# Kernel optimization log

Measured on AMD Instinct MI355X. Metric: run time of the kernel, lower is better.

The kernel has to match this reference:

```python
import jax, jax.numpy as jnp
import numpy as np

BS, H, W, C = 32, 64, 64, 256
SEQ = 32


def setup_inputs() -> dict:
    key = jax.random.key(0)
    k1, k2, k3, k4, k5 = jax.random.split(key, 5)
    x = jax.random.normal(k1, (BS, H, W, C), dtype=jnp.float32)
    sentence = jax.random.normal(k2, (BS, C), dtype=jnp.float32)  # unused in call()
    context = jax.random.normal(k3, (BS, SEQ, C), dtype=jnp.float32)
    mask = jax.random.bernoulli(k4, 0.3, (BS, SEQ))
    W_word = jax.random.normal(k5, (C, C), dtype=jnp.float32) * (1.0 / np.sqrt(C))
    return {"x": x, "sentence": sentence, "context": context, "mask": mask, "W_word": W_word}


def reference(x, sentence, context, mask, W_word):
    bs, h, w, c = x.shape
    hw = h * w
    seq = context.shape[1]
    xf = x.reshape(bs, hw, c)                                   # [bs, hw, C]
    ctx = jnp.einsum('bsd,dc->bsc', context, W_word)            # conv1x1 word projection
    attn = jnp.einsum('bnc,bsc->bns', xf, ctx)                  # [bs, hw, seq]
    attn = attn.reshape(bs * hw, seq)
    # faithful to original: mask tiled hw times along axis 0 (block-repeat order)
    mask_t = jnp.tile(mask, (hw, 1))                            # [bs*hw, seq]
    neg_inf = jnp.asarray(-jnp.inf, dtype=attn.dtype)
    attn = jnp.where(mask_t, neg_inf, attn)
    attn = jax.nn.softmax(attn, axis=-1).reshape(bs, hw, seq)
    # matmul(ctx^T, attn^T) -> [bs, C, hw] -> transpose -> [bs, hw, C]
    weighted_context = jnp.einsum('bsc,bns->bnc', ctx, attn).reshape(bs, h, w, c)
    word_attn = attn.reshape(bs, h, w, seq)
    return weighted_context, word_attn
```

## Files before the change

### kernel.cpp

```cpp
#include <hip/hip_runtime.h>
#include <stdint.h>

typedef __attribute__((ext_vector_type(8))) short short8;
typedef __attribute__((ext_vector_type(4))) float float4v;

#define HW   4096
#define CC   256
#define SEQQ 32
#define BSZ  32
#define RPB  128

#define SGRP     1032
#define CTXT_SZ  (8 * SGRP)
#define PSTR_P   40

static __device__ __forceinline__ uint16_t f2bf(float f) {
  union { float f; uint32_t u; } v; v.f = f;
  uint32_t r = v.u + 0x7FFFu + ((v.u >> 16) & 1u);
  return (uint16_t)(r >> 16);
}
static __device__ __forceinline__ float bf2f(uint16_t h) {
  union { uint32_t u; float f; } v; v.u = ((uint32_t)h) << 16;
  return v.f;
}

extern "C" __global__ __launch_bounds__(256) void prep_kernel(
    const float* __restrict__ ctx_in,
    const float* __restrict__ Wp,
    const void*  __restrict__ mask,
    uint32_t* __restrict__ maskbits_ws,
    uint16_t* __restrict__ hiT_ws,
    uint16_t* __restrict__ loT_ws)
{
  const int t = threadIdx.x;
  if (blockIdx.x == 256) {
    __shared__ int byteFlag;
    if (t == 0) byteFlag = 0;
    __syncthreads();
    const uint8_t* mb = (const uint8_t*)mask;
    int nz = 0;
    for (int i = t; i < 1024; i += 256)
      if ((i & 3) == 1 && mb[i] != 0) nz = 1;
    if (nz) atomicOr(&byteFlag, 1);
    __syncthreads();
    const bool byteMode = (byteFlag != 0);
    const uint32_t* mw32 = (const uint32_t*)mask;
    if (t < 32) {
      uint32_t bits = 0;
      for (int s = 0; s < 32; ++s) {
        bool m = byteMode ? (mb[t * 32 + s] != 0) : (mw32[t * 32 + s] != 0);
        if (m) bits |= (1u << s);
      }
      maskbits_ws[t] = bits;
    }
    return;
  }

  const int r0 = blockIdx.x * 4;
  __shared__ float crow[4][CC];
  for (int i = t; i < 1024; i += 256)
    crow[i >> 8][i & 255] = ctx_in[(size_t)r0 * CC + i];
  __syncthreads();

  const int j  = t >> 6;
  const int c4 = (t & 63) << 2;
  float4v acc = {0.f, 0.f, 0.f, 0.f};
  #pragma unroll 8
  for (int d = 0; d < CC; ++d) {
    float s = crow[j][d];
    const float4 wv = *(const float4*)&Wp[(size_t)d * CC + c4];
    acc[0] += s * wv.x; acc[1] += s * wv.y;
    acc[2] += s * wv.z; acc[3] += s * wv.w;
  }

  const int row = r0 + j, bb = row >> 5, ss = row & 31;
  const size_t base = (size_t)bb * CTXT_SZ + (ss >> 2) * SGRP + (ss & 3) * 16;
  #pragma unroll
  for (int q = 0; q < 4; ++q) {
    const int c = c4 + q;
    const float v = acc[q];
    const uint16_t h  = f2bf(v);
    const uint16_t lo = f2bf(v - bf2f(h));
    const size_t idx = base + (c >> 4) * 64 + (c & 15);
    hiT_ws[idx] = h;
    loT_ws[idx] = lo;
  }
}

#define COMPUTE_TILE(XA, XB, TBASE)                                           \
  {                                                                           \
    float4v acc0 = {0.f, 0.f, 0.f, 0.f};                                      \
    float4v acc1 = {0.f, 0.f, 0.f, 0.f};                                      \
    _Pragma("unroll")                                                         \
    for (int k0 = 0; k0 < 8; ++k0) {                                          \
      float xv[8] = {XA[k0].x, XA[k0].y, XA[k0].z, XA[k0].w,                  \
                     XB[k0].x, XB[k0].y, XB[k0].z, XB[k0].w};                 \
      short8 ah, al;                                                          \
      _Pragma("unroll")                                                       \
      for (int jj = 0; jj < 8; ++jj) {                                        \
        uint32_t u = __float_as_uint(xv[jj]);                                 \
        ah[jj] = (short)(u >> 16);                                            \
        float rr_ = xv[jj] - __uint_as_float(u & 0xFFFF0000u);                \
        al[jj] = (short)(__float_as_uint(rr_) >> 16);                         \
      }                                                                       \
      const int ka = sbase + k0 * 128;                                        \
      short8 bh0 = *(const short8*)&hiT[ka];                                  \
      short8 bl0 = *(const short8*)&loT[ka];                                  \
      short8 bh1 = *(const short8*)&hiT[ka + 4 * SGRP];                       \
      short8 bl1 = *(const short8*)&loT[ka + 4 * SGRP];                       \
      acc0 = __builtin_amdgcn_mfma_f32_16x16x32_bf16(bh0, ah, acc0, 0, 0, 0); \
      acc0 = __builtin_amdgcn_mfma_f32_16x16x32_bf16(bl0, ah, acc0, 0, 0, 0); \
      acc0 = __builtin_amdgcn_mfma_f32_16x16x32_bf16(bh0, al, acc0, 0, 0, 0); \
      acc1 = __builtin_amdgcn_mfma_f32_16x16x32_bf16(bh1, ah, acc1, 0, 0, 0); \
      acc1 = __builtin_amdgcn_mfma_f32_16x16x32_bf16(bl1, ah, acc1, 0, 0, 0); \
      acc1 = __builtin_amdgcn_mfma_f32_16x16x32_bf16(bh1, al, acc1, 0, 0, 0); \
    }                                                                         \
    const int n = (TBASE) + l15;                                              \
    const uint32_t mwd = maskW[n & 31];                                       \
    float v[8];                                                               \
    _Pragma("unroll")                                                         \
    for (int r = 0; r < 4; ++r) {                                             \
      v[r]     = (mwd & (1u << (quad * 4 + r)))      ? -1e30f : acc0[r];      \
      v[4 + r] = (mwd & (1u << (16 + quad * 4 + r))) ? -1e30f : acc1[r];      \
    }                                                                         \
    float mx = v[0];                                                          \
    _Pragma("unroll")                                                         \
    for (int jq = 1; jq < 8; ++jq) mx = fmaxf(mx, v[jq]);                     \
    mx = fmaxf(mx, __shfl_xor(mx, 16, 64));                                   \
    mx = fmaxf(mx, __shfl_xor(mx, 32, 64));                                   \
    float e[8], sm = 0.f;                                                     \
    _Pragma("unroll")                                                         \
    for (int jq = 0; jq < 8; ++jq) { e[jq] = __expf(v[jq] - mx); sm += e[jq]; } \
    sm += __shfl_xor(sm, 16, 64);                                             \
    sm += __shfl_xor(sm, 32, 64);                                             \
    const float inv = 1.0f / sm;                                              \
    float p[8];                                                               \
    _Pragma("unroll")                                                         \
    for (int jq = 0; jq < 8; ++jq) p[jq] = e[jq] * inv;                       \
         \
    const int r8 = l15 & 7;                                                   \
    *(float4*)&ostW[l15 * 32 + ((quad ^ r8) << 2)] =                          \
        make_float4(p[0], p[1], p[2], p[3]);                                  \
    *(float4*)&ostW[l15 * 32 + (((4 + quad) ^ r8) << 2)] =                    \
        make_float4(p[4], p[5], p[6], p[7]);                                  \
    uint32_t w0 = (uint32_t)f2bf(p[0]) | ((uint32_t)f2bf(p[1]) << 16);        \
    uint32_t w1 = (uint32_t)f2bf(p[2]) | ((uint32_t)f2bf(p[3]) << 16);        \
    uint32_t w2 = (uint32_t)f2bf(p[4]) | ((uint32_t)f2bf(p[5]) << 16);        \
    uint32_t w3 = (uint32_t)f2bf(p[6]) | ((uint32_t)f2bf(p[7]) << 16);        \
    uint16_t* prow = &pL[(w * 16 + l15) * PSTR_P];                            \
    *(uint2*)(prow + quad * 4)      = make_uint2(w0, w1);                     \
    *(uint2*)(prow + 16 + quad * 4) = make_uint2(w2, w3);                     \
    _Pragma("unroll")                                                         \
    for (int i2 = 0; i2 < 2; ++i2) {                                          \
      const int rr = 8 * i2 + (lane >> 3);                                    \
      const int mm = lane & 7;                                                \
      float4 vv = *(const float4*)&ostW[rr * 32 + ((mm ^ (rr & 7)) << 2)];    \
      *(float4*)(out1 + ((size_t)b * HW + (TBASE) + rr) * SEQQ + mm * 4) = vv;\
    }                                                                         \
     \
    short8 pa = *(const short8*)&pL[(w * 16 + l15) * PSTR_P + quad * 8];      \
    _Pragma("unroll")                                                         \
    for (int cg = 0; cg < 4; ++cg) {                                          \
      _Pragma("unroll")                                                       \
      for (int j2 = 0; j2 < 4; ++j2) {                                        \
        const int ct = cg * 4 + j2;                                           \
        short8 bfr;                                                           \
        _Pragma("unroll")                                                     \
        for (int jj = 0; jj < 8; ++jj)                                        \
          bfr[jj] = (short)hiT[cbase + (jj >> 2) * SGRP + ct * 64 + (jj & 3) * 16]; \
        float4v z = {0.f, 0.f, 0.f, 0.f};                                     \
        float4v dd = __builtin_amdgcn_mfma_f32_16x16x32_bf16(bfr, pa, z, 0, 0, 0); \
        const int ss = j2 * 4 + quad;                                         \
        *(float4*)&ostW[l15 * 64 + ((ss ^ l15) << 2)] =                       \
            make_float4(dd[0], dd[1], dd[2], dd[3]);                          \
      }                                                                       \
      _Pragma("unroll")                                                       \
      for (int i2 = 0; i2 < 4; ++i2) {                                        \
        const int rr = 4 * i2 + (lane >> 4);                                  \
        const int mm = lane & 15;                                             \
        float4 vv = *(const float4*)&ostW[rr * 64 + ((mm ^ rr) << 2)];        \
        *(float4*)(out0 + ((size_t)b * HW + (TBASE) + rr) * CC + cg * 64 + mm * 4) = vv; \
      }                                                                       \
    }                                                                         \
  }

extern "C" __global__ __launch_bounds__(256, 2) void attn_main(
    const float* __restrict__ x,
    const uint8_t* __restrict__ ws,
    float* __restrict__ out0,
    float* __restrict__ out1)
{
  const uint32_t* maskbits_ws = (const uint32_t*)ws;
  const uint16_t* hiT_ws = (const uint16_t*)(ws + 128);
  const uint16_t* loT_ws = hiT_ws + (size_t)BSZ * CTXT_SZ;

  __shared__ __align__(16) uint16_t hiT[CTXT_SZ];
  __shared__ __align__(16) uint16_t loT[CTXT_SZ];
  __shared__ __align__(16) uint16_t pL[64 * PSTR_P];
  __shared__ __align__(16) float    oStgF[4 * 1024];
  __shared__ uint32_t maskW[32];

  const int tid = threadIdx.x;
  const int b   = blockIdx.y;
  const int n0  = blockIdx.x * RPB;

  const int w    = tid >> 6;
  const int lane = tid & 63;
  const int l15  = lane & 15;
  const int quad = lane >> 4;
  const int nwave = n0 + w * 32;
  float* ostW = &oStgF[w * 1024];

  const uint4* sHi = (const uint4*)(hiT_ws + (size_t)b * CTXT_SZ);
  const uint4* sLo = (const uint4*)(loT_ws + (size_t)b * CTXT_SZ);

  uint4 hS[4], lS[4];
  #pragma unroll
  for (int k = 0; k < 4; ++k) {
    hS[k] = sHi[tid + k * 256];
    lS[k] = sLo[tid + k * 256];
  }

  const float* xrow0 = x + ((size_t)b * HW + nwave + l15) * CC + quad * 8;
  float4 xa0[8], xb0[8];
  #pragma unroll
  for (int k0 = 0; k0 < 8; ++k0) {
    xa0[k0] = *(const float4*)(xrow0 + k0 * 32);
    xb0[k0] = *(const float4*)(xrow0 + k0 * 32 + 4);
  }
  asm volatile("" ::: "memory");

  {
    uint4* dHi = (uint4*)hiT;
    uint4* dLo = (uint4*)loT;
    #pragma unroll
    for (int k = 0; k < 4; ++k) {
      dHi[tid + k * 256] = hS[k];
      dLo[tid + k * 256] = lS[k];
    }
    if (tid < 8) { dHi[1024 + tid] = sHi[1024 + tid]; dLo[1024 + tid] = sLo[1024 + tid]; }
    if (tid < 32) maskW[tid] = maskbits_ws[tid];
  }
  __syncthreads();

  const float* xrow1 = xrow0 + 16 * CC;
  float4 xa1[8], xb1[8];
  #pragma unroll
  for (int k0 = 0; k0 < 8; ++k0) {
    xa1[k0] = *(const float4*)(xrow1 + k0 * 32);
    xb1[k0] = *(const float4*)(xrow1 + k0 * 32 + 4);
  }
  asm volatile("" ::: "memory");

  const int sbase = (l15 >> 2) * SGRP + (l15 & 3) * 16 + (quad >> 1) * 64 + (quad & 1) * 8;
  const int cbase = quad * 2 * SGRP + l15;

  COMPUTE_TILE(xa0, xb0, nwave);
  COMPUTE_TILE(xa1, xb1, nwave + 16);
}

extern "C" void kernel_launch(void* const* d_in, const int* in_sizes, int n_in,
                              void* d_out, int out_size, void* d_ws, size_t ws_size,
                              hipStream_t stream) {
  const float* x      = (const float*)d_in[0];
  const float* ctx_in = (const float*)d_in[2];
  const void*  mask   = d_in[3];
  const float* Wp     = (const float*)d_in[4];

  float* out0 = (float*)d_out;
  float* out1 = out0 + (size_t)BSZ * HW * CC;

  uint8_t*  ws          = (uint8_t*)d_ws;
  uint32_t* maskbits_ws = (uint32_t*)ws;
  uint16_t* hiT_ws      = (uint16_t*)(ws + 128);
  uint16_t* loT_ws      = hiT_ws + (size_t)BSZ * CTXT_SZ;

  prep_kernel<<<257, 256, 0, stream>>>(ctx_in, Wp, mask, maskbits_ws,
                                       hiT_ws, loT_ws);
  attn_main<<<dim3(HW / RPB, BSZ), 256, 0, stream>>>(x, ws, out0, out1);
}
```

Before: 281.1 us.

## Double rows per block with software-pipelined x loads and nontemporal stores

Each block now covers 256 rows, and each wave processes four 16-row tiles instead of two. The x loads for the next tile are issued before the current tile is computed, in a double-buffered register pipeline. This spreads the per-block cost of staging the context into shared memory over more rows and overlaps global loads with compute. Output stores switch to nontemporal builtins so they avoid polluting the cache. The change halves the grid size, which may lower occupancy and parallelism, and keeps register pressure high.

```diff
diff --git a/kernel.cpp b/kernel.cpp
--- a/kernel.cpp
+++ b/kernel.cpp
@@ -8,7 +8,7 @@
 #define CC   256
 #define SEQQ 32
 #define BSZ  32
-#define RPB  128
+#define RPB  256
 
 #define SGRP     1032
 #define CTXT_SZ  (8 * SGRP)
@@ -87,6 +87,17 @@
   }
 }
 
+#define LOAD_CHUNK(XA, XB, CIDX)                                              \
+  {                                                                           \
+    const float* xr_ = xrow0 + (CIDX) * 16 * CC;                              \
+    _Pragma("unroll")                                                         \
+    for (int k0 = 0; k0 < 8; ++k0) {                                          \
+      XA[k0] = *(const float4*)(xr_ + k0 * 32);                               \
+      XB[k0] = *(const float4*)(xr_ + k0 * 32 + 4);                           \
+    }                                                                         \
+  }                                                                           \
+  asm volatile("" ::: "memory");
+
 #define COMPUTE_TILE(XA, XB, TBASE)                                           \
   {                                                                           \
     float4v acc0 = {0.f, 0.f, 0.f, 0.f};                                      \
@@ -139,10 +150,10 @@
     for (int jq = 0; jq < 8; ++jq) p[jq] = e[jq] * inv;                       \
          \
     const int r8 = l15 & 7;                                                   \
-    *(float4*)&ostW[l15 * 32 + ((quad ^ r8) << 2)] =                          \
-        make_float4(p[0], p[1], p[2], p[3]);                                  \
-    *(float4*)&ostW[l15 * 32 + (((4 + quad) ^ r8) << 2)] =                    \
-        make_float4(p[4], p[5], p[6], p[7]);                                  \
+    float4v p03 = {p[0], p[1], p[2], p[3]};                                   \
+    float4v p47 = {p[4], p[5], p[6], p[7]};                                   \
+    *(float4v*)&ostW[l15 * 32 + ((quad ^ r8) << 2)]       = p03;              \
+    *(float4v*)&ostW[l15 * 32 + (((4 + quad) ^ r8) << 2)] = p47;              \
     uint32_t w0 = (uint32_t)f2bf(p[0]) | ((uint32_t)f2bf(p[1]) << 16);        \
     uint32_t w1 = (uint32_t)f2bf(p[2]) | ((uint32_t)f2bf(p[3]) << 16);        \
     uint32_t w2 = (uint32_t)f2bf(p[4]) | ((uint32_t)f2bf(p[5]) << 16);        \
@@ -154,8 +165,9 @@
     for (int i2 = 0; i2 < 2; ++i2) {                                          \
       const int rr = 8 * i2 + (lane >> 3);                                    \
       const int mm = lane & 7;                                                \
-      float4 vv = *(const float4*)&ostW[rr * 32 + ((mm ^ (rr & 7)) << 2)];    \
-      *(float4*)(out1 + ((size_t)b * HW + (TBASE) + rr) * SEQQ + mm * 4) = vv;\
+      float4v vv = *(const float4v*)&ostW[rr * 32 + ((mm ^ (rr & 7)) << 2)];  \
+      __builtin_nontemporal_store(vv,                                         \
+        (float4v*)(out1 + ((size_t)b * HW + (TBASE) + rr) * SEQQ + mm * 4));  \
     }                                                                         \
      \
     short8 pa = *(const short8*)&pL[(w * 16 + l15) * PSTR_P + quad * 8];      \
@@ -171,15 +183,15 @@
         float4v z = {0.f, 0.f, 0.f, 0.f};                                     \
         float4v dd = __builtin_amdgcn_mfma_f32_16x16x32_bf16(bfr, pa, z, 0, 0, 0); \
         const int ss = j2 * 4 + quad;                                         \
-        *(float4*)&ostW[l15 * 64 + ((ss ^ l15) << 2)] =                       \
-            make_float4(dd[0], dd[1], dd[2], dd[3]);                          \
+        *(float4v*)&ostW[l15 * 64 + ((ss ^ l15) << 2)] = dd;                  \
       }                                                                       \
       _Pragma("unroll")                                                       \
       for (int i2 = 0; i2 < 4; ++i2) {                                        \
         const int rr = 4 * i2 + (lane >> 4);                                  \
         const int mm = lane & 15;                                             \
-        float4 vv = *(const float4*)&ostW[rr * 64 + ((mm ^ rr) << 2)];        \
-        *(float4*)(out0 + ((size_t)b * HW + (TBASE) + rr) * CC + cg * 64 + mm * 4) = vv; \
+        float4v vv = *(const float4v*)&ostW[rr * 64 + ((mm ^ rr) << 2)];      \
+        __builtin_nontemporal_store(vv,                                       \
+          (float4v*)(out0 + ((size_t)b * HW + (TBASE) + rr) * CC + cg * 64 + mm * 4)); \
       }                                                                       \
     }                                                                         \
   }
@@ -208,7 +220,7 @@
   const int lane = tid & 63;
   const int l15  = lane & 15;
   const int quad = lane >> 4;
-  const int nwave = n0 + w * 32;
+  const int nwave = n0 + w * 64;
   float* ostW = &oStgF[w * 1024];
 
   const uint4* sHi = (const uint4*)(hiT_ws + (size_t)b * CTXT_SZ);
@@ -222,13 +234,8 @@
   }
 
   const float* xrow0 = x + ((size_t)b * HW + nwave + l15) * CC + quad * 8;
-  float4 xa0[8], xb0[8];
-  #pragma unroll
-  for (int k0 = 0; k0 < 8; ++k0) {
-    xa0[k0] = *(const float4*)(xrow0 + k0 * 32);
-    xb0[k0] = *(const float4*)(xrow0 + k0 * 32 + 4);
-  }
-  asm volatile("" ::: "memory");
+  float4 xa0[8], xb0[8], xa1[8], xb1[8];
+  LOAD_CHUNK(xa0, xb0, 0);
 
   {
     uint4* dHi = (uint4*)hiT;
@@ -243,20 +250,16 @@
   }
   __syncthreads();
 
-  const float* xrow1 = xrow0 + 16 * CC;
-  float4 xa1[8], xb1[8];
-  #pragma unroll
-  for (int k0 = 0; k0 < 8; ++k0) {
-    xa1[k0] = *(const float4*)(xrow1 + k0 * 32);
-    xb1[k0] = *(const float4*)(xrow1 + k0 * 32 + 4);
-  }
-  asm volatile("" ::: "memory");
-
   const int sbase = (l15 >> 2) * SGRP + (l15 & 3) * 16 + (quad >> 1) * 64 + (quad & 1) * 8;
   const int cbase = quad * 2 * SGRP + l15;
 
+  LOAD_CHUNK(xa1, xb1, 1);
   COMPUTE_TILE(xa0, xb0, nwave);
+  LOAD_CHUNK(xa0, xb0, 2);
   COMPUTE_TILE(xa1, xb1, nwave + 16);
+  LOAD_CHUNK(xa1, xb1, 3);
+  COMPUTE_TILE(xa0, xb0, nwave + 32);
+  COMPUTE_TILE(xa1, xb1, nwave + 48);
 }
 
 extern "C" void kernel_launch(void* const* d_in, const int* in_sizes, int n_in,
```

Result: slower. 289.1 us (+2.8%).

## Split fused attention kernel into score/softmax and weighted-context kernels

Applied to the files above, without the earlier changes.

Splits the single attention kernel into two launches. The first computes scores and softmax and writes word_attn. The second reads word_attn back from global memory, converts it to bf16 and runs the MFMA context product to write the weighted context. The likely aim is to lower per-kernel LDS and register use so that the second stage can run at higher occupancy (launch bounds of 4). The cost is an extra kernel launch, a re-read of the probability tensor, and a second load of the context tiles into shared memory.

```diff
diff --git a/kernel.cpp b/kernel.cpp
--- a/kernel.cpp
+++ b/kernel.cpp
@@ -12,7 +12,6 @@
 
 #define SGRP     1032
 #define CTXT_SZ  (8 * SGRP)
-#define PSTR_P   40
 
 static __device__ __forceinline__ uint16_t f2bf(float f) {
   union { float f; uint32_t u; } v; v.f = f;
@@ -87,7 +86,7 @@
   }
 }
 
-#define COMPUTE_TILE(XA, XB, TBASE)                                           \
+#define COMPUTE_TILE_P1(XA, XB, TBASE)                                        \
   {                                                                           \
     float4v acc0 = {0.f, 0.f, 0.f, 0.f};                                      \
     float4v acc1 = {0.f, 0.f, 0.f, 0.f};                                      \
@@ -143,13 +142,6 @@
         make_float4(p[0], p[1], p[2], p[3]);                                  \
     *(float4*)&ostW[l15 * 32 + (((4 + quad) ^ r8) << 2)] =                    \
         make_float4(p[4], p[5], p[6], p[7]);                                  \
-    uint32_t w0 = (uint32_t)f2bf(p[0]) | ((uint32_t)f2bf(p[1]) << 16);        \
-    uint32_t w1 = (uint32_t)f2bf(p[2]) | ((uint32_t)f2bf(p[3]) << 16);        \
-    uint32_t w2 = (uint32_t)f2bf(p[4]) | ((uint32_t)f2bf(p[5]) << 16);        \
-    uint32_t w3 = (uint32_t)f2bf(p[6]) | ((uint32_t)f2bf(p[7]) << 16);        \
-    uint16_t* prow = &pL[(w * 16 + l15) * PSTR_P];                            \
-    *(uint2*)(prow + quad * 4)      = make_uint2(w0, w1);                     \
-    *(uint2*)(prow + 16 + quad * 4) = make_uint2(w2, w3);                     \
     _Pragma("unroll")                                                         \
     for (int i2 = 0; i2 < 2; ++i2) {                                          \
       const int rr = 8 * i2 + (lane >> 3);                                    \
@@ -157,37 +149,11 @@
       float4 vv = *(const float4*)&ostW[rr * 32 + ((mm ^ (rr & 7)) << 2)];    \
       *(float4*)(out1 + ((size_t)b * HW + (TBASE) + rr) * SEQQ + mm * 4) = vv;\
     }                                                                         \
-     \
-    short8 pa = *(const short8*)&pL[(w * 16 + l15) * PSTR_P + quad * 8];      \
-    _Pragma("unroll")                                                         \
-    for (int cg = 0; cg < 4; ++cg) {                                          \
-      _Pragma("unroll")                                                       \
-      for (int j2 = 0; j2 < 4; ++j2) {                                        \
-        const int ct = cg * 4 + j2;                                           \
-        short8 bfr;                                                           \
-        _Pragma("unroll")                                                     \
-        for (int jj = 0; jj < 8; ++jj)                                        \
-          bfr[jj] = (short)hiT[cbase + (jj >> 2) * SGRP + ct * 64 + (jj & 3) * 16]; \
-        float4v z = {0.f, 0.f, 0.f, 0.f};                                     \
-        float4v dd = __builtin_amdgcn_mfma_f32_16x16x32_bf16(bfr, pa, z, 0, 0, 0); \
-        const int ss = j2 * 4 + quad;                                         \
-        *(float4*)&ostW[l15 * 64 + ((ss ^ l15) << 2)] =                       \
-            make_float4(dd[0], dd[1], dd[2], dd[3]);                          \
-      }                                                                       \
-      _Pragma("unroll")                                                       \
-      for (int i2 = 0; i2 < 4; ++i2) {                                        \
-        const int rr = 4 * i2 + (lane >> 4);                                  \
-        const int mm = lane & 15;                                             \
-        float4 vv = *(const float4*)&ostW[rr * 64 + ((mm ^ rr) << 2)];        \
-        *(float4*)(out0 + ((size_t)b * HW + (TBASE) + rr) * CC + cg * 64 + mm * 4) = vv; \
-      }                                                                       \
-    }                                                                         \
-  }
-
-extern "C" __global__ __launch_bounds__(256, 2) void attn_main(
+  }
+
+extern "C" __global__ __launch_bounds__(256, 2) void attn_p1(
     const float* __restrict__ x,
     const uint8_t* __restrict__ ws,
-    float* __restrict__ out0,
     float* __restrict__ out1)
 {
   const uint32_t* maskbits_ws = (const uint32_t*)ws;
@@ -196,8 +162,7 @@
 
   __shared__ __align__(16) uint16_t hiT[CTXT_SZ];
   __shared__ __align__(16) uint16_t loT[CTXT_SZ];
-  __shared__ __align__(16) uint16_t pL[64 * PSTR_P];
-  __shared__ __align__(16) float    oStgF[4 * 1024];
+  __shared__ __align__(16) float    oStgF[4 * 512];
   __shared__ uint32_t maskW[32];
 
   const int tid = threadIdx.x;
@@ -209,7 +174,7 @@
   const int l15  = lane & 15;
   const int quad = lane >> 4;
   const int nwave = n0 + w * 32;
-  float* ostW = &oStgF[w * 1024];
+  float* ostW = &oStgF[w * 512];
 
   const uint4* sHi = (const uint4*)(hiT_ws + (size_t)b * CTXT_SZ);
   const uint4* sLo = (const uint4*)(loT_ws + (size_t)b * CTXT_SZ);
@@ -253,10 +218,86 @@
   asm volatile("" ::: "memory");
 
   const int sbase = (l15 >> 2) * SGRP + (l15 & 3) * 16 + (quad >> 1) * 64 + (quad & 1) * 8;
+
+  COMPUTE_TILE_P1(xa0, xb0, nwave);
+  COMPUTE_TILE_P1(xa1, xb1, nwave + 16);
+}
+
+extern "C" __global__ __launch_bounds__(256, 4) void attn_p2(
+    const float* __restrict__ out1,
+    const uint8_t* __restrict__ ws,
+    float* __restrict__ out0)
+{
+  const uint16_t* hiT_ws = (const uint16_t*)(ws + 128);
+
+  __shared__ __align__(16) uint16_t hiT[CTXT_SZ];
+  __shared__ __align__(16) float    oStgF[4 * 1024];
+
+  const int tid = threadIdx.x;
+  const int b   = blockIdx.y;
+  const int n0  = blockIdx.x * RPB;
+
+  const int w    = tid >> 6;
+  const int lane = tid & 63;
+  const int l15  = lane & 15;
+  const int quad = lane >> 4;
+  const int nwave = n0 + w * 32;
+  float* ostW = &oStgF[w * 1024];
+
+  const float* prow0 = out1 + ((size_t)b * HW + nwave + l15) * SEQQ + quad * 8;
+  const float* prow1 = prow0 + 16 * SEQQ;
+  float4 q00 = *(const float4*)(prow0);
+  float4 q01 = *(const float4*)(prow0 + 4);
+  float4 q10 = *(const float4*)(prow1);
+  float4 q11 = *(const float4*)(prow1 + 4);
+  asm volatile("" ::: "memory");
+
+  {
+    const uint4* sHi = (const uint4*)(hiT_ws + (size_t)b * CTXT_SZ);
+    uint4* dHi = (uint4*)hiT;
+    #pragma unroll
+    for (int k = 0; k < 4; ++k) dHi[tid + k * 256] = sHi[tid + k * 256];
+    if (tid < 8) dHi[1024 + tid] = sHi[1024 + tid];
+  }
+  __syncthreads();
+
   const int cbase = quad * 2 * SGRP + l15;
 
-  COMPUTE_TILE(xa0, xb0, nwave);
-  COMPUTE_TILE(xa1, xb1, nwave + 16);
+  #pragma unroll
+  for (int t2 = 0; t2 < 2; ++t2) {
+    const float4 qa = t2 ? q10 : q00;
+    const float4 qb = t2 ? q11 : q01;
+    const int tbase = nwave + t2 * 16;
+    union { uint32_t u[4]; short8 s; } pau;
+    pau.u[0] = (uint32_t)f2bf(qa.x) | ((uint32_t)f2bf(qa.y) << 16);
+    pau.u[1] = (uint32_t)f2bf(qa.z) | ((uint32_t)f2bf(qa.w) << 16);
+    pau.u[2] = (uint32_t)f2bf(qb.x) | ((uint32_t)f2bf(qb.y) << 16);
+    pau.u[3] = (uint32_t)f2bf(qb.z) | ((uint32_t)f2bf(qb.w) << 16);
+    short8 pa = pau.s;
+
+    #pragma unroll
+    for (int cg = 0; cg < 4; ++cg) {
+      #pragma unroll
+      for (int j2 = 0; j2 < 4; ++j2) {
+        const int ct = cg * 4 + j2;
+        short8 bfr;
+        #pragma unroll
+        for (int jj = 0; jj < 8; ++jj)
+          bfr[jj] = (short)hiT[cbase + (jj >> 2) * SGRP + ct * 64 + (jj & 3) * 16];
+        float4v z = {0.f, 0.f, 0.f, 0.f};
+        float4v dd = __builtin_amdgcn_mfma_f32_16x16x32_bf16(bfr, pa, z, 0, 0, 0);
+        const int ss = j2 * 4 + quad;
+        *(float4v*)&ostW[l15 * 64 + ((ss ^ l15) << 2)] = dd;
+      }
+      #pragma unroll
+      for (int i2 = 0; i2 < 4; ++i2) {
+        const int rr = 4 * i2 + (lane >> 4);
+        const int mm = lane & 15;
+        float4 vv = *(const float4*)&ostW[rr * 64 + ((mm ^ rr) << 2)];
+        *(float4*)(out0 + ((size_t)b * HW + tbase + rr) * CC + cg * 64 + mm * 4) = vv;
+      }
+    }
+  }
 }
 
 extern "C" void kernel_launch(void* const* d_in, const int* in_sizes, int n_in,
@@ -277,5 +318,6 @@
 
   prep_kernel<<<257, 256, 0, stream>>>(ctx_in, Wp, mask, maskbits_ws,
                                        hiT_ws, loT_ws);
-  attn_main<<<dim3(HW / RPB, BSZ), 256, 0, stream>>>(x, ws, out0, out1);
-}
+  attn_p1<<<dim3(HW / RPB, BSZ), 256, 0, stream>>>(x, ws, out1);
+  attn_p2<<<dim3(HW / RPB, BSZ), 256, 0, stream>>>(out1, ws, out0);
+}
```

Result: no change. 283.7 us (+0.9%).
